# Kernel optimization log

Measured on AMD Instinct MI355X. Metric: run time of the kernel, lower is better.

## Reference

```python
import jax, jax.numpy as jnp
import numpy as np

B, S, D = 2, 2048, 1024
H, DK, DV = 16, 64, 64


def setup_inputs() -> dict:
    key = jax.random.key(0)
    ks = jax.random.split(key, 11)
    s = 1.0 / np.sqrt(D)
    inp = {
        "Q": jax.random.normal(ks[0], (B, S, D), jnp.float32),
        "K": jax.random.normal(ks[1], (B, S, D), jnp.float32),
        "V": jax.random.normal(ks[2], (B, S, D), jnp.float32),
        "Wq": jax.random.normal(ks[3], (H, D, DK), jnp.float32) * s,
        "bq": jax.random.normal(ks[4], (H, DK), jnp.float32) * 0.01,
        "Wk": jax.random.normal(ks[5], (H, D, DK), jnp.float32) * s,
        "bk": jax.random.normal(ks[6], (H, DK), jnp.float32) * 0.01,
        "Wv": jax.random.normal(ks[7], (H, D, DV), jnp.float32) * s,
        "bv": jax.random.normal(ks[8], (H, DV), jnp.float32) * 0.01,
        "Wm": jax.random.normal(ks[9], (H * DV, D), jnp.float32) * (1.0 / np.sqrt(H * DV)),
        "bm": jax.random.normal(ks[10], (D,), jnp.float32) * 0.01,
    }
    return inp


def reference(Q, K, V, Wq, bq, Wk, bk, Wv, bv, Wm, bm):
    # Per-head projections (batched over heads instead of a Python loop)
    q = jnp.einsum("bqd,hdk->bhqk", Q, Wq) + bq[None, :, None, :]   # [B,H,S,DK]
    k = jnp.einsum("bsd,hdk->bhsk", K, Wk) + bk[None, :, None, :]   # [B,H,S,DK]
    v = jnp.einsum("bsd,hdv->bhsv", V, Wv) + bv[None, :, None, :]   # [B,H,S,DV]
    scores = jnp.einsum("bhqk,bhsk->bhqs", q, k) / jnp.sqrt(jnp.asarray(DK, q.dtype))
    attn = jax.nn.softmax(scores, axis=-1)                           # [B,H,S,S]
    ctx = jnp.einsum("bhqs,bhsv->bhqv", attn, v)                     # [B,H,S,DV]
    # Concat heads along feature dim, then output projection
    stacked_ctx = jnp.transpose(ctx, (0, 2, 1, 3)).reshape(B, S, H * DV)
    multi_head = stacked_ctx @ Wm + bm                               # [B,S,D]
    # torch.cat(attn_weights_list, dim=-1): [B, S, H*S]
    stacked_attention_weights = jnp.transpose(attn, (0, 2, 1, 3)).reshape(B, S, H * S)
    return multi_head, stacked_attention_weights
```

## Files before the change

### kernel.cpp

```cpp
#include <hip/hip_runtime.h>

#define B_ 2
#define S_ 2048
#define D_ 1024
#define H_ 16
#define M_ 4096

typedef unsigned short u16;
typedef unsigned int u32;
typedef short bf8 __attribute__((ext_vector_type(8)));
typedef float f4 __attribute__((ext_vector_type(4)));

#define MFMA16(a, b, c) __builtin_amdgcn_mfma_f32_16x16x32_bf16(a, b, c, 0, 0, 0)

__device__ __forceinline__ u16 f2b(float f) {
  u32 u = __builtin_bit_cast(u32, f);
  u += 0x7fffu + ((u >> 16) & 1);
  return (u16)(u >> 16);
}
__device__ __forceinline__ u32 pack2(float lo, float hi) {
  return (u32)f2b(lo) | ((u32)f2b(hi) << 16);
}
__device__ __forceinline__ float b2f(u16 h) {
  return __builtin_bit_cast(float, (u32)h << 16);
}

__device__ __forceinline__ void stage64(u16* lds, const u16* __restrict__ src,
                                        int srcStride, int t) {
#pragma unroll
  for (int i = 0; i < 2; ++i) {
    int c = t + 256 * i;
    int row = c >> 3, col = c & 7;
    uint4 v = *(const uint4*)(src + (size_t)row * srcStride + col * 8);
    int dcol = col ^ (row & 7);
    *(uint4*)(lds + row * 64 + dcol * 8) = v;
  }
}

__device__ __forceinline__ bf8 ldA(const u16* lds, int rowBase, int kc, int lane) {
  int row = rowBase + (lane & 15);
  int c = (kc * 4 + (lane >> 4)) ^ (row & 7);
  return *(const bf8*)(lds + row * 64 + c * 8);
}

__global__ __launch_bounds__(256) void cvtk(const float* __restrict__ in,
                                            u16* __restrict__ out, int n) {
  int i = (blockIdx.x * 256 + threadIdx.x) * 8;
  if (i >= n) return;
  float4 a = *(const float4*)(in + i);
  float4 b = *(const float4*)(in + i + 4);
  uint4 o;
  o.x = pack2(a.x, a.y);
  o.y = pack2(a.z, a.w);
  o.z = pack2(b.x, b.y);
  o.w = pack2(b.z, b.w);
  *(uint4*)(out + i) = o;
}

__global__ __launch_bounds__(256) void tcvt(const float* __restrict__ in,
                                            u16* __restrict__ out, int R, int C) {
  int rt = blockIdx.x, ct = blockIdx.y, z = blockIdx.z;
  in += (size_t)z * R * C;
  out += (size_t)z * R * C;
  __shared__ float tile[64][65];
  int t = threadIdx.x;
  int r = t >> 2, cc = (t & 3) * 16;
#pragma unroll
  for (int j = 0; j < 16; j += 4) {
    float4 v = *(const float4*)(in + (size_t)(rt * 64 + r) * C + ct * 64 + cc + j);
    tile[r][cc + j] = v.x;
    tile[r][cc + j + 1] = v.y;
    tile[r][cc + j + 2] = v.z;
    tile[r][cc + j + 3] = v.w;
  }
  __syncthreads();
  int c = t >> 2;
  u32 buf[8];
#pragma unroll
  for (int j = 0; j < 8; ++j)
    buf[j] = pack2(tile[cc + 2 * j][c], tile[cc + 2 * j + 1][c]);
  uint4* dst = (uint4*)(out + (size_t)(ct * 64 + c) * R + rt * 64 + cc);
  dst[0] = make_uint4(buf[0], buf[1], buf[2], buf[3]);
  dst[1] = make_uint4(buf[4], buf[5], buf[6], buf[7]);
}

__global__ __launch_bounds__(256) void tb16(const u16* __restrict__ in,
                                            u16* __restrict__ out) {
  int st = blockIdx.x, z = blockIdx.z;
  in += (size_t)z * S_ * 64;
  out += (size_t)z * 64 * S_;
  __shared__ u16 tile[64][72];
  int t = threadIdx.x;
#pragma unroll
  for (int i = 0; i < 2; ++i) {
    int c = t + 256 * i;
    int row = c >> 3, col = (c & 7) * 8;
    uint4 v = *(const uint4*)(in + (size_t)(st * 64 + row) * 64 + col);
    *(uint4*)&tile[row][col] = v;
  }
  __syncthreads();
  int dv = t >> 2, cc = (t & 3) * 16;
  u32 buf[8];
#pragma unroll
  for (int j = 0; j < 8; ++j) {
    u16 a = tile[cc + 2 * j][dv];
    u16 b = tile[cc + 2 * j + 1][dv];
    buf[j] = (u32)a | ((u32)b << 16);
  }
  uint4* dst = (uint4*)(out + (size_t)dv * S_ + st * 64 + cc);
  dst[0] = make_uint4(buf[0], buf[1], buf[2], buf[3]);
  dst[1] = make_uint4(buf[4], buf[5], buf[6], buf[7]);
}

__global__ __launch_bounds__(256) void proj_k(const u16* __restrict__ A,
                                              const u16* __restrict__ BT,
                                              const float* __restrict__ bias,
                                              u16* __restrict__ outp, float scale) {
  int mt = blockIdx.x, h = blockIdx.y;
  int t = threadIdx.x, lane = t & 63, w = t >> 6;
  int quad = lane >> 4, col = lane & 15;
  __shared__ u16 Asm[64 * 64], Bsm[64 * 64];
  f4 acc[4] = {};
  const u16* Abase = A + (size_t)(mt * 64) * 1024;
  const u16* Bbase = BT + (size_t)h * 64 * 1024;
  for (int kt = 0; kt < 16; ++kt) {
    __syncthreads();
    stage64(Asm, Abase + kt * 64, 1024, t);
    stage64(Bsm, Bbase + kt * 64, 1024, t);
    __syncthreads();
    bf8 a0 = ldA(Asm, w * 16, 0, lane);
    bf8 a1 = ldA(Asm, w * 16, 1, lane);
#pragma unroll
    for (int nf = 0; nf < 4; ++nf) {
      bf8 b0 = ldA(Bsm, nf * 16, 0, lane);
      bf8 b1 = ldA(Bsm, nf * 16, 1, lane);
      acc[nf] = MFMA16(a0, b0, acc[nf]);
      acc[nf] = MFMA16(a1, b1, acc[nf]);
    }
  }
#pragma unroll
  for (int nf = 0; nf < 4; ++nf) {
    int n = nf * 16 + col;
    float bs = bias[h * 64 + n];
#pragma unroll
    for (int r = 0; r < 4; ++r) {
      int gm = mt * 64 + w * 16 + quad * 4 + r;
      int bb = gm >> 11, s = gm & 2047;
      outp[(size_t)((bb * H_ + h) * S_ + s) * 64 + n] = f2b((acc[nf][r] + bs) * scale);
    }
  }
}

__global__ __launch_bounds__(256) void gemmo(const u16* __restrict__ A,
                                             const u16* __restrict__ BT,
                                             const float* __restrict__ bias,
                                             float* __restrict__ outp) {
  int mt = blockIdx.x, nt = blockIdx.y;
  int t = threadIdx.x, lane = t & 63, w = t >> 6;
  int quad = lane >> 4, col = lane & 15;
  __shared__ u16 Asm[64 * 64], Bsm[64 * 64];
  f4 acc[4] = {};
  for (int kt = 0; kt < 16; ++kt) {
    __syncthreads();
    stage64(Asm, A + (size_t)(mt * 64) * 1024 + kt * 64, 1024, t);
    stage64(Bsm, BT + (size_t)(nt * 64) * 1024 + kt * 64, 1024, t);
    __syncthreads();
    bf8 a0 = ldA(Asm, w * 16, 0, lane);
    bf8 a1 = ldA(Asm, w * 16, 1, lane);
#pragma unroll
    for (int nf = 0; nf < 4; ++nf) {
      bf8 b0 = ldA(Bsm, nf * 16, 0, lane);
      bf8 b1 = ldA(Bsm, nf * 16, 1, lane);
      acc[nf] = MFMA16(a0, b0, acc[nf]);
      acc[nf] = MFMA16(a1, b1, acc[nf]);
    }
  }
#pragma unroll
  for (int nf = 0; nf < 4; ++nf) {
    int n = nt * 64 + nf * 16 + col;
    float bs = bias[n];
#pragma unroll
    for (int r = 0; r < 4; ++r) {
      int gm = mt * 64 + w * 16 + quad * 4 + r;
      outp[(size_t)gm * 1024 + n] = acc[nf][r] + bs;
    }
  }
}

__device__ __forceinline__ void qk_tile(const u16* Ksm, bf8 qf0, bf8 qf1, int lane,
                                        f4 sc[4]) {
#pragma unroll
  for (int fr = 0; fr < 4; ++fr) {
    bf8 k0 = ldA(Ksm, fr * 16, 0, lane);
    bf8 k1 = ldA(Ksm, fr * 16, 1, lane);
    sc[fr] = MFMA16(k0, qf0, sc[fr]);
    sc[fr] = MFMA16(k1, qf1, sc[fr]);
  }
}

__global__ __launch_bounds__(256) void attn_k(const u16* __restrict__ qp,
                                              const u16* __restrict__ kp,
                                              const u16* __restrict__ vT,
                                              u16* __restrict__ ctxo,
                                              float* __restrict__ attw) {
  int qt = blockIdx.x, h = blockIdx.y, b = blockIdx.z;
  int t = threadIdx.x, lane = t & 63, w = t >> 6;
  int quad = lane >> 4, col = lane & 15;
  __shared__ u16 Qsm[64 * 64], Ksm[64 * 64], Vsm[64 * 64];
  __shared__ u16 Psm[4][16 * 64];

  const u16* qbase = qp + ((size_t)(b * H_ + h) * S_ + qt * 64) * 64;
  const u16* kbase = kp + (size_t)(b * H_ + h) * S_ * 64;
  const u16* vbase = vT + (size_t)(b * H_ + h) * 64 * S_;

  stage64(Qsm, qbase, 64, t);
  __syncthreads();
  bf8 qf0 = ldA(Qsm, w * 16, 0, lane);
  bf8 qf1 = ldA(Qsm, w * 16, 1, lane);

  float m = -1e30f, l = 0.f;
  for (int kt = 0; kt < 32; ++kt) {
    __syncthreads();
    stage64(Ksm, kbase + (size_t)kt * 64 * 64, 64, t);
    __syncthreads();
    f4 sc[4] = {};
    qk_tile(Ksm, qf0, qf1, lane, sc);
    float mx = -1e30f;
#pragma unroll
    for (int fr = 0; fr < 4; ++fr)
#pragma unroll
      for (int r = 0; r < 4; ++r) mx = fmaxf(mx, sc[fr][r]);
    if (mx > m) {
      l *= __expf(m - mx);
      m = mx;
    }
    float ssum = 0.f;
#pragma unroll
    for (int fr = 0; fr < 4; ++fr)
#pragma unroll
      for (int r = 0; r < 4; ++r) ssum += __expf(sc[fr][r] - m);
    l += ssum;
  }
#pragma unroll
  for (int off = 16; off <= 32; off <<= 1) {
    float mo = __shfl_xor(m, off);
    float lo = __shfl_xor(l, off);
    float mn = fmaxf(m, mo);
    l = l * __expf(m - mn) + lo * __expf(mo - mn);
    m = mn;
  }
  float linv = 1.f / l;

  f4 ctxa[4] = {};
  u16* Pw = Psm[w];
  size_t awbase = ((size_t)(b * S_ + qt * 64 + w * 16) * H_ + h) * S_;
  for (int kt = 0; kt < 32; ++kt) {
    __syncthreads();
    stage64(Ksm, kbase + (size_t)kt * 64 * 64, 64, t);
    stage64(Vsm, vbase + kt * 64, S_, t);
    __syncthreads();
    f4 sc[4] = {};
    qk_tile(Ksm, qf0, qf1, lane, sc);
#pragma unroll
    for (int fr = 0; fr < 4; ++fr) {
      float p0 = __expf(sc[fr][0] - m) * linv;
      float p1 = __expf(sc[fr][1] - m) * linv;
      float p2 = __expf(sc[fr][2] - m) * linv;
      float p3 = __expf(sc[fr][3] - m) * linv;
      int bo = col * 128 + ((fr * 32 + quad * 8) ^ ((col & 7) << 4));
      uint2 u;
      u.x = pack2(p0, p1);
      u.y = pack2(p2, p3);
      *(uint2*)((char*)Pw + bo) = u;
    }
    bf8 pf0 = ldA(Pw, 0, 0, lane);
    bf8 pf1 = ldA(Pw, 0, 1, lane);
#pragma unroll
    for (int fr = 0; fr < 4; ++fr) {
      bf8 v0 = ldA(Vsm, fr * 16, 0, lane);
      bf8 v1 = ldA(Vsm, fr * 16, 1, lane);
      ctxa[fr] = MFMA16(v0, pf0, ctxa[fr]);
      ctxa[fr] = MFMA16(v1, pf1, ctxa[fr]);
    }
#pragma unroll
    for (int it = 0; it < 2; ++it) {
      int q = (lane >> 3) + 8 * it;
      int c16 = lane & 7;
      int bo = q * 128 + ((c16 ^ (q & 7)) << 4);
      bf8 pv = *(const bf8*)((const char*)Pw + bo);
      float* dst = attw + awbase + (size_t)q * (H_ * S_) + kt * 64 + c16 * 8;
      float4 o0, o1;
      o0.x = b2f((u16)pv[0]);
      o0.y = b2f((u16)pv[1]);
      o0.z = b2f((u16)pv[2]);
      o0.w = b2f((u16)pv[3]);
      o1.x = b2f((u16)pv[4]);
      o1.y = b2f((u16)pv[5]);
      o1.z = b2f((u16)pv[6]);
      o1.w = b2f((u16)pv[7]);
      *(float4*)dst = o0;
      *((float4*)dst + 1) = o1;
    }
  }
  int qg = qt * 64 + w * 16 + col;
  size_t cb = ((size_t)(b * S_ + qg) * H_ + h) * 64;
#pragma unroll
  for (int fr = 0; fr < 4; ++fr) {
    uint2 u;
    u.x = pack2(ctxa[fr][0], ctxa[fr][1]);
    u.y = pack2(ctxa[fr][2], ctxa[fr][3]);
    *(uint2*)(ctxo + cb + fr * 16 + quad * 4) = u;
  }
}

extern "C" void kernel_launch(void* const* d_in, const int* in_sizes, int n_in,
                              void* d_out, int out_size, void* d_ws, size_t ws_size,
                              hipStream_t stream) {
  const float* Q = (const float*)d_in[0];
  const float* K = (const float*)d_in[1];
  const float* V = (const float*)d_in[2];
  const float* Wq = (const float*)d_in[3];
  const float* bq = (const float*)d_in[4];
  const float* Wk = (const float*)d_in[5];
  const float* bk = (const float*)d_in[6];
  const float* Wv = (const float*)d_in[7];
  const float* bv = (const float*)d_in[8];
  const float* Wm = (const float*)d_in[9];
  const float* bm = (const float*)d_in[10];
  float* out0 = (float*)d_out;
  float* out1 = out0 + (size_t)M_ * D_;

  u16* X = (u16*)d_ws;
  u16* WT = X + 4194304;
  u16* qp = WT + 1048576;
  u16* kp = qp + 4194304;
  u16* vp = kp + 4194304;
  u16* vTp = vp + 4194304;
  (void)in_sizes; (void)n_in; (void)out_size; (void)ws_size;

  const int NQKV = M_ * D_;

  cvtk<<<2048, 256, 0, stream>>>(Q, X, NQKV);
  tcvt<<<dim3(16, 1, 16), 256, 0, stream>>>(Wq, WT, 1024, 64);
  proj_k<<<dim3(64, 16), 256, 0, stream>>>(X, WT, bq, qp, 0.125f);
  cvtk<<<2048, 256, 0, stream>>>(K, X, NQKV);
  tcvt<<<dim3(16, 1, 16), 256, 0, stream>>>(Wk, WT, 1024, 64);
  proj_k<<<dim3(64, 16), 256, 0, stream>>>(X, WT, bk, kp, 1.0f);
  cvtk<<<2048, 256, 0, stream>>>(V, X, NQKV);
  tcvt<<<dim3(16, 1, 16), 256, 0, stream>>>(Wv, WT, bv ? WT != nullptr ? 1024 : 1024 : 1024, 64);
  proj_k<<<dim3(64, 16), 256, 0, stream>>>(X, WT, bv, vp, 1.0f);
  tb16<<<dim3(32, 1, 32), 256, 0, stream>>>(vp, vTp);
  attn_k<<<dim3(32, 16, 2), 256, 0, stream>>>(qp, kp, vTp, vp, out1);
  tcvt<<<dim3(16, 16, 1), 256, 0, stream>>>(Wm, WT, 1024, 1024);
  gemmo<<<dim3(64, 16), 256, 0, stream>>>(vp, WT, bm, out0);
}
```

Before: 339.9 us.

## Fuse fp32-to-bf16 conversion into 128x128 GEMMs and load attention operands directly

Drops the separate activation conversion kernels by converting fp32 inputs to bf16 while staging tiles inside a new templated 128x128 GEMM. That GEMM is used for the Q/K/V projections and the output projection, in place of the 64x64 tiles. The attention kernel now loads Q, K and V fragments straight from global memory into registers instead of staging through LDS with block barriers. It also remaps block indices so consecutive blocks are spread across heads. The intent is to cut extra passes over memory, kernel launches and sync overhead, at the cost of higher register pressure, redundant global loads across waves and possibly uncoalesced fragment reads.

Result: slower. 553.4 us (+62.8%).

```diff
diff --git a/kernel.cpp b/kernel.cpp
--- a/kernel.cpp
+++ b/kernel.cpp
@@ -24,18 +24,7 @@
 __device__ __forceinline__ float b2f(u16 h) {
   return __builtin_bit_cast(float, (u32)h << 16);
 }
-
-__device__ __forceinline__ void stage64(u16* lds, const u16* __restrict__ src,
-                                        int srcStride, int t) {
-#pragma unroll
-  for (int i = 0; i < 2; ++i) {
-    int c = t + 256 * i;
-    int row = c >> 3, col = c & 7;
-    uint4 v = *(const uint4*)(src + (size_t)row * srcStride + col * 8);
-    int dcol = col ^ (row & 7);
-    *(uint4*)(lds + row * 64 + dcol * 8) = v;
-  }
-}
+__device__ __forceinline__ bf8 g16(const u16* p) { return *(const bf8*)p; }
 
 __device__ __forceinline__ bf8 ldA(const u16* lds, int rowBase, int kc, int lane) {
   int row = rowBase + (lane & 15);
@@ -43,18 +32,33 @@
   return *(const bf8*)(lds + row * 64 + c * 8);
 }
 
-__global__ __launch_bounds__(256) void cvtk(const float* __restrict__ in,
-                                            u16* __restrict__ out, int n) {
-  int i = (blockIdx.x * 256 + threadIdx.x) * 8;
-  if (i >= n) return;
-  float4 a = *(const float4*)(in + i);
-  float4 b = *(const float4*)(in + i + 4);
-  uint4 o;
-  o.x = pack2(a.x, a.y);
-  o.y = pack2(a.z, a.w);
-  o.z = pack2(b.x, b.y);
-  o.w = pack2(b.z, b.w);
-  *(uint4*)(out + i) = o;
+__device__ __forceinline__ void stageB(u16* lds, const u16* __restrict__ src,
+                                       int srcStride, int t) {
+#pragma unroll
+  for (int i = 0; i < 4; ++i) {
+    int c = t + 256 * i;
+    int row = c >> 3, col = c & 7;
+    uint4 v = *(const uint4*)(src + (size_t)row * srcStride + col * 8);
+    *(uint4*)(lds + row * 64 + (col ^ (row & 7)) * 8) = v;
+  }
+}
+
+__device__ __forceinline__ void stageAf(u16* lds, const float* __restrict__ src,
+                                        int srcStride, int t) {
+#pragma unroll
+  for (int i = 0; i < 4; ++i) {
+    int c = t + 256 * i;
+    int row = c >> 3, col = c & 7;
+    const float* p = src + (size_t)row * srcStride + col * 8;
+    float4 a = *(const float4*)p;
+    float4 b = *(const float4*)(p + 4);
+    uint4 o;
+    o.x = pack2(a.x, a.y);
+    o.y = pack2(a.z, a.w);
+    o.z = pack2(b.x, b.y);
+    o.w = pack2(b.z, b.w);
+    *(uint4*)(lds + row * 64 + (col ^ (row & 7)) * 8) = o;
+  }
 }
 
 __global__ __launch_bounds__(256) void tcvt(const float* __restrict__ in,
@@ -112,126 +116,99 @@
   dst[1] = make_uint4(buf[4], buf[5], buf[6], buf[7]);
 }
 
-__global__ __launch_bounds__(256) void proj_k(const u16* __restrict__ A,
-                                              const u16* __restrict__ BT,
-                                              const float* __restrict__ bias,
-                                              u16* __restrict__ outp, float scale) {
-  int mt = blockIdx.x, h = blockIdx.y;
+template <int AF32, int SCATTER>
+__global__ __launch_bounds__(256) void gemm128(const void* __restrict__ Ap,
+                                               const u16* __restrict__ BT,
+                                               const float* __restrict__ bias,
+                                               void* __restrict__ outp, float scale) {
+  int mt = blockIdx.x, nt = blockIdx.y;
+  int t = threadIdx.x, lane = t & 63, w = t >> 6;
+  int wr = w >> 1, wc = w & 1;
+  int quad = lane >> 4, col = lane & 15;
+  __shared__ u16 Asm[128 * 64], Bsm[128 * 64];
+  f4 acc[4][4] = {};
+  for (int kt = 0; kt < 16; ++kt) {
+    __syncthreads();
+    if (AF32)
+      stageAf(Asm, (const float*)Ap + (size_t)(mt * 128) * 1024 + kt * 64, 1024, t);
+    else
+      stageB(Asm, (const u16*)Ap + (size_t)(mt * 128) * 1024 + kt * 64, 1024, t);
+    stageB(Bsm, BT + (size_t)(nt * 128) * 1024 + kt * 64, 1024, t);
+    __syncthreads();
+#pragma unroll
+    for (int kc = 0; kc < 2; ++kc) {
+      bf8 a[4], b[4];
+#pragma unroll
+      for (int fr = 0; fr < 4; ++fr) a[fr] = ldA(Asm, wr * 64 + fr * 16, kc, lane);
+#pragma unroll
+      for (int nf = 0; nf < 4; ++nf) b[nf] = ldA(Bsm, wc * 64 + nf * 16, kc, lane);
+#pragma unroll
+      for (int fr = 0; fr < 4; ++fr)
+#pragma unroll
+        for (int nf = 0; nf < 4; ++nf)
+          acc[fr][nf] = MFMA16(a[fr], b[nf], acc[fr][nf]);
+    }
+  }
+#pragma unroll
+  for (int fr = 0; fr < 4; ++fr)
+#pragma unroll
+    for (int nf = 0; nf < 4; ++nf) {
+      int n = nt * 128 + wc * 64 + nf * 16 + col;
+      float bs = bias[n];
+#pragma unroll
+      for (int r = 0; r < 4; ++r) {
+        int gm = mt * 128 + wr * 64 + fr * 16 + quad * 4 + r;
+        if (SCATTER) {
+          int h = n >> 6, d = n & 63;
+          int bb = gm >> 11, s = gm & 2047;
+          ((u16*)outp)[(size_t)((bb * H_ + h) * S_ + s) * 64 + d] =
+              f2b((acc[fr][nf][r] + bs) * scale);
+        } else {
+          ((float*)outp)[(size_t)gm * 1024 + n] = acc[fr][nf][r] + bs;
+        }
+      }
+    }
+}
+
+__global__ __launch_bounds__(256) void attn2(const u16* __restrict__ qp,
+                                             const u16* __restrict__ kp,
+                                             const u16* __restrict__ vT,
+                                             u16* __restrict__ ctxo,
+                                             float* __restrict__ attw) {
+  int bid = blockIdx.x;
+  int l = (bid & 7) * 128 + (bid >> 3);
+  int qt = l & 31, hb = l >> 5;
+  int h = hb & 15, b = hb >> 4;
   int t = threadIdx.x, lane = t & 63, w = t >> 6;
   int quad = lane >> 4, col = lane & 15;
-  __shared__ u16 Asm[64 * 64], Bsm[64 * 64];
-  f4 acc[4] = {};
-  const u16* Abase = A + (size_t)(mt * 64) * 1024;
-  const u16* Bbase = BT + (size_t)h * 64 * 1024;
-  for (int kt = 0; kt < 16; ++kt) {
-    __syncthreads();
-    stage64(Asm, Abase + kt * 64, 1024, t);
-    stage64(Bsm, Bbase + kt * 64, 1024, t);
-    __syncthreads();
-    bf8 a0 = ldA(Asm, w * 16, 0, lane);
-    bf8 a1 = ldA(Asm, w * 16, 1, lane);
-#pragma unroll
-    for (int nf = 0; nf < 4; ++nf) {
-      bf8 b0 = ldA(Bsm, nf * 16, 0, lane);
-      bf8 b1 = ldA(Bsm, nf * 16, 1, lane);
-      acc[nf] = MFMA16(a0, b0, acc[nf]);
-      acc[nf] = MFMA16(a1, b1, acc[nf]);
-    }
-  }
-#pragma unroll
-  for (int nf = 0; nf < 4; ++nf) {
-    int n = nf * 16 + col;
-    float bs = bias[h * 64 + n];
-#pragma unroll
-    for (int r = 0; r < 4; ++r) {
-      int gm = mt * 64 + w * 16 + quad * 4 + r;
-      int bb = gm >> 11, s = gm & 2047;
-      outp[(size_t)((bb * H_ + h) * S_ + s) * 64 + n] = f2b((acc[nf][r] + bs) * scale);
-    }
-  }
-}
-
-__global__ __launch_bounds__(256) void gemmo(const u16* __restrict__ A,
-                                             const u16* __restrict__ BT,
-                                             const float* __restrict__ bias,
-                                             float* __restrict__ outp) {
-  int mt = blockIdx.x, nt = blockIdx.y;
-  int t = threadIdx.x, lane = t & 63, w = t >> 6;
-  int quad = lane >> 4, col = lane & 15;
-  __shared__ u16 Asm[64 * 64], Bsm[64 * 64];
-  f4 acc[4] = {};
-  for (int kt = 0; kt < 16; ++kt) {
-    __syncthreads();
-    stage64(Asm, A + (size_t)(mt * 64) * 1024 + kt * 64, 1024, t);
-    stage64(Bsm, BT + (size_t)(nt * 64) * 1024 + kt * 64, 1024, t);
-    __syncthreads();
-    bf8 a0 = ldA(Asm, w * 16, 0, lane);
-    bf8 a1 = ldA(Asm, w * 16, 1, lane);
-#pragma unroll
-    for (int nf = 0; nf < 4; ++nf) {
-      bf8 b0 = ldA(Bsm, nf * 16, 0, lane);
-      bf8 b1 = ldA(Bsm, nf * 16, 1, lane);
-      acc[nf] = MFMA16(a0, b0, acc[nf]);
-      acc[nf] = MFMA16(a1, b1, acc[nf]);
-    }
-  }
-#pragma unroll
-  for (int nf = 0; nf < 4; ++nf) {
-    int n = nt * 64 + nf * 16 + col;
-    float bs = bias[n];
-#pragma unroll
-    for (int r = 0; r < 4; ++r) {
-      int gm = mt * 64 + w * 16 + quad * 4 + r;
-      outp[(size_t)gm * 1024 + n] = acc[nf][r] + bs;
-    }
-  }
-}
-
-__device__ __forceinline__ void qk_tile(const u16* Ksm, bf8 qf0, bf8 qf1, int lane,
-                                        f4 sc[4]) {
-#pragma unroll
-  for (int fr = 0; fr < 4; ++fr) {
-    bf8 k0 = ldA(Ksm, fr * 16, 0, lane);
-    bf8 k1 = ldA(Ksm, fr * 16, 1, lane);
-    sc[fr] = MFMA16(k0, qf0, sc[fr]);
-    sc[fr] = MFMA16(k1, qf1, sc[fr]);
-  }
-}
-
-__global__ __launch_bounds__(256) void attn_k(const u16* __restrict__ qp,
-                                              const u16* __restrict__ kp,
-                                              const u16* __restrict__ vT,
-                                              u16* __restrict__ ctxo,
-                                              float* __restrict__ attw) {
-  int qt = blockIdx.x, h = blockIdx.y, b = blockIdx.z;
-  int t = threadIdx.x, lane = t & 63, w = t >> 6;
-  int quad = lane >> 4, col = lane & 15;
-  __shared__ u16 Qsm[64 * 64], Ksm[64 * 64], Vsm[64 * 64];
   __shared__ u16 Psm[4][16 * 64];
 
-  const u16* qbase = qp + ((size_t)(b * H_ + h) * S_ + qt * 64) * 64;
   const u16* kbase = kp + (size_t)(b * H_ + h) * S_ * 64;
   const u16* vbase = vT + (size_t)(b * H_ + h) * 64 * S_;
-
-  stage64(Qsm, qbase, 64, t);
-  __syncthreads();
-  bf8 qf0 = ldA(Qsm, w * 16, 0, lane);
-  bf8 qf1 = ldA(Qsm, w * 16, 1, lane);
-
-  float m = -1e30f, l = 0.f;
+  const u16* qrow = qp + ((size_t)(b * H_ + h) * S_ + qt * 64 + w * 16) * 64;
+  int r16 = (lane & 15) * 64;
+  int c0 = (lane >> 4) * 8, c1 = c0 + 32;
+  bf8 qf0 = g16(qrow + r16 + c0);
+  bf8 qf1 = g16(qrow + r16 + c1);
+
+  float m = -1e30f, l_ = 0.f;
   for (int kt = 0; kt < 32; ++kt) {
-    __syncthreads();
-    stage64(Ksm, kbase + (size_t)kt * 64 * 64, 64, t);
-    __syncthreads();
+    const u16* kb = kbase + kt * 64 * 64;
     f4 sc[4] = {};
-    qk_tile(Ksm, qf0, qf1, lane, sc);
+#pragma unroll
+    for (int fr = 0; fr < 4; ++fr) {
+      bf8 k0 = g16(kb + fr * 16 * 64 + r16 + c0);
+      bf8 k1 = g16(kb + fr * 16 * 64 + r16 + c1);
+      sc[fr] = MFMA16(k0, qf0, sc[fr]);
+      sc[fr] = MFMA16(k1, qf1, sc[fr]);
+    }
     float mx = -1e30f;
 #pragma unroll
     for (int fr = 0; fr < 4; ++fr)
 #pragma unroll
       for (int r = 0; r < 4; ++r) mx = fmaxf(mx, sc[fr][r]);
     if (mx > m) {
-      l *= __expf(m - mx);
+      l_ *= __expf(m - mx);
       m = mx;
     }
     float ssum = 0.f;
@@ -239,28 +216,38 @@
     for (int fr = 0; fr < 4; ++fr)
 #pragma unroll
       for (int r = 0; r < 4; ++r) ssum += __expf(sc[fr][r] - m);
-    l += ssum;
+    l_ += ssum;
   }
 #pragma unroll
   for (int off = 16; off <= 32; off <<= 1) {
     float mo = __shfl_xor(m, off);
-    float lo = __shfl_xor(l, off);
+    float lo = __shfl_xor(l_, off);
     float mn = fmaxf(m, mo);
-    l = l * __expf(m - mn) + lo * __expf(mo - mn);
+    l_ = l_ * __expf(m - mn) + lo * __expf(mo - mn);
     m = mn;
   }
-  float linv = 1.f / l;
+  float linv = 1.f / l_;
 
   f4 ctxa[4] = {};
   u16* Pw = Psm[w];
   size_t awbase = ((size_t)(b * S_ + qt * 64 + w * 16) * H_ + h) * S_;
   for (int kt = 0; kt < 32; ++kt) {
-    __syncthreads();
-    stage64(Ksm, kbase + (size_t)kt * 64 * 64, 64, t);
-    stage64(Vsm, vbase + kt * 64, S_, t);
-    __syncthreads();
+    const u16* kb = kbase + kt * 64 * 64;
     f4 sc[4] = {};
-    qk_tile(Ksm, qf0, qf1, lane, sc);
+#pragma unroll
+    for (int fr = 0; fr < 4; ++fr) {
+      bf8 k0 = g16(kb + fr * 16 * 64 + r16 + c0);
+      bf8 k1 = g16(kb + fr * 16 * 64 + r16 + c1);
+      sc[fr] = MFMA16(k0, qf0, sc[fr]);
+      sc[fr] = MFMA16(k1, qf1, sc[fr]);
+    }
+    bf8 v0[4], v1[4];
+#pragma unroll
+    for (int fr = 0; fr < 4; ++fr) {
+      const u16* vb = vbase + (size_t)(fr * 16 + (lane & 15)) * S_ + kt * 64;
+      v0[fr] = g16(vb + c0);
+      v1[fr] = g16(vb + c1);
+    }
 #pragma unroll
     for (int fr = 0; fr < 4; ++fr) {
       float p0 = __expf(sc[fr][0] - m) * linv;
@@ -277,10 +264,8 @@
     bf8 pf1 = ldA(Pw, 0, 1, lane);
 #pragma unroll
     for (int fr = 0; fr < 4; ++fr) {
-      bf8 v0 = ldA(Vsm, fr * 16, 0, lane);
-      bf8 v1 = ldA(Vsm, fr * 16, 1, lane);
-      ctxa[fr] = MFMA16(v0, pf0, ctxa[fr]);
-      ctxa[fr] = MFMA16(v1, pf1, ctxa[fr]);
+      ctxa[fr] = MFMA16(v0[fr], pf0, ctxa[fr]);
+      ctxa[fr] = MFMA16(v1[fr], pf1, ctxa[fr]);
     }
 #pragma unroll
     for (int it = 0; it < 2; ++it) {
@@ -329,28 +314,25 @@
   const float* bm = (const float*)d_in[10];
   float* out0 = (float*)d_out;
   float* out1 = out0 + (size_t)M_ * D_;
-
-  u16* X = (u16*)d_ws;
-  u16* WT = X + 4194304;
-  u16* qp = WT + 1048576;
+  (void)in_sizes; (void)n_in; (void)out_size; (void)ws_size;
+
+  u16* WT0 = (u16*)d_ws;
+  u16* WT1 = WT0 + 1048576;
+  u16* WT2 = WT1 + 1048576;
+  u16* WT3 = WT2 + 1048576;
+  u16* qp = WT3 + 1048576;
   u16* kp = qp + 4194304;
   u16* vp = kp + 4194304;
   u16* vTp = vp + 4194304;
-  (void)in_sizes; (void)n_in; (void)out_size; (void)ws_size;
-
-  const int NQKV = M_ * D_;
-
-  cvtk<<<2048, 256, 0, stream>>>(Q, X, NQKV);
-  tcvt<<<dim3(16, 1, 16), 256, 0, stream>>>(Wq, WT, 1024, 64);
-  proj_k<<<dim3(64, 16), 256, 0, stream>>>(X, WT, bq, qp, 0.125f);
-  cvtk<<<2048, 256, 0, stream>>>(K, X, NQKV);
-  tcvt<<<dim3(16, 1, 16), 256, 0, stream>>>(Wk, WT, 1024, 64);
-  proj_k<<<dim3(64, 16), 256, 0, stream>>>(X, WT, bk, kp, 1.0f);
-  cvtk<<<2048, 256, 0, stream>>>(V, X, NQKV);
-  tcvt<<<dim3(16, 1, 16), 256, 0, stream>>>(Wv, WT, bv ? WT != nullptr ? 1024 : 1024 : 1024, 64);
-  proj_k<<<dim3(64, 16), 256, 0, stream>>>(X, WT, bv, vp, 1.0f);
+
+  tcvt<<<dim3(16, 1, 16), 256, 0, stream>>>(Wq, WT0, 1024, 64);
+  tcvt<<<dim3(16, 1, 16), 256, 0, stream>>>(Wk, WT1, 1024, 64);
+  tcvt<<<dim3(16, 1, 16), 256, 0, stream>>>(Wv, WT2, 1024, 64);
+  tcvt<<<dim3(16, 16, 1), 256, 0, stream>>>(Wm, WT3, 1024, 1024);
+  gemm128<1, 1><<<dim3(32, 8), 256, 0, stream>>>(Q, WT0, bq, qp, 0.125f);
+  gemm128<1, 1><<<dim3(32, 8), 256, 0, stream>>>(K, WT1, bk, kp, 1.0f);
+  gemm128<1, 1><<<dim3(32, 8), 256, 0, stream>>>(V, WT2, bv, vp, 1.0f);
   tb16<<<dim3(32, 1, 32), 256, 0, stream>>>(vp, vTp);
-  attn_k<<<dim3(32, 16, 2), 256, 0, stream>>>(qp, kp, vTp, vp, out1);
-  tcvt<<<dim3(16, 16, 1), 256, 0, stream>>>(Wm, WT, 1024, 1024);
-  gemmo<<<dim3(64, 16), 256, 0, stream>>>(vp, WT, bm, out0);
-}
+  attn2<<<1024, 256, 0, stream>>>(qp, kp, vTp, vp, out1);
+  gemm128<0, 0><<<dim3(32, 8), 256, 0, stream>>>(vp, WT3, bm, out0, 1.0f);
+}
```
